# Kernel tuning notes

Hardware: AMD Instinct MI355X
Metric: run time of the kernel (lower is better)

The kernel has to match this reference:

```python
import jax, jax.numpy as jnp
import numpy as np

B, T, ENC_IN, C_OUT = 128, 100, 38, 38
D_MODEL, H, L, D_FF = 512, 8, 3, 512
D_VAE, D_MC, D_C, K = 128, 64, 64, 50
OT_EPS = 0.1

def _ln(x, g, b):
    m = x.mean(-1, keepdims=True)
    v = ((x - m) ** 2).mean(-1, keepdims=True)
    return (x - m) / jnp.sqrt(v + 1e-5) * g + b

def _pos_emb(t, d):
    pos = jnp.arange(t, dtype=jnp.float32)[:, None]
    div = jnp.exp(jnp.arange(0, d, 2, dtype=jnp.float32) * (-np.log(10000.0) / d))
    pe = jnp.zeros((t, d), jnp.float32)
    return pe.at[:, 0::2].set(jnp.sin(pos * div)).at[:, 1::2].set(jnp.cos(pos * div))

def _forward(x, emb_w, Wq, Wk, Wv, Wo, bq, bk, bv, bo, c1w, c1b, c2w, c2b,
             ln1g, ln1b, ln2g, ln2b, lnfg, lnfb, en2de_w, en2de_b,
             eh1w, eh1b, eh2w, eh2b, mamw, mamb, malvw, malvb,
             zmw, zmb, zlvw, zlvb, dzm1w, dzm1b, dzm2w, dzm2b,
             dzl1w, dzl1b, dzl2w, dzl2b, dxm1w, dxm1b, dxm2w, dxm2b,
             otw, otb, theta, projw, projb):
    b, t, _ = x.shape
    # DataEmbedding: circular Conv1d(k=3) token embedding + sinusoidal positions
    xp = jnp.pad(x, ((0, 0), (1, 1), (0, 0)), mode='wrap')
    h = jax.lax.conv_general_dilated(xp, emb_w, (1,), 'VALID',
                                     dimension_numbers=('NWC', 'WIO', 'NWC'))
    h = h + _pos_emb(t, h.shape[-1])[None]
    series_list = []
    scale = 1.0 / jnp.sqrt(jnp.float32(D_MODEL // H))
    for l in range(L):
        q = (h @ Wq[l] + bq[l]).reshape(b, t, H, -1)
        k = (h @ Wk[l] + bk[l]).reshape(b, t, H, -1)
        v = (h @ Wv[l] + bv[l]).reshape(b, t, H, -1)
        # AnomalyAttention series-association: softmax(scale * Q K^T)
        series = jax.nn.softmax(jnp.einsum('bthd,bshd->bhts', q, k) * scale, axis=-1)
        o = jnp.einsum('bhts,bshd->bthd', series, v).reshape(b, t, -1) @ Wo[l] + bo[l]
        h = _ln(h + o, ln1g[l], ln1b[l])
        # conv1d(k=1) FFN == per-token linear; torch weight layout [out, in]
        y = jax.nn.gelu(h @ c1w[l].T + c1b[l], approximate=False) @ c2w[l].T + c2b[l]
        h = _ln(h + y, ln2g[l], ln2b[l])
        series_list.append(series)
    h = _ln(h, lnfg, lnfb)          # encoder final norm
    h = h @ en2de_w + en2de_b       # en2de: [B,T,d_vae]
    # Decoder (eval-mode reparameterization: z = mean)
    h1 = h @ eh1w + eh1b
    h2 = h1 @ eh2w + eh2b
    ma_mean = h2 @ mamw + mamb
    ma_logvar = h2 @ malvw + malvb
    ma = ma_mean
    hb = jnp.concatenate([h1, ma], axis=-1)
    z_mean = hb @ zmw + zmb
    z_logvar = hb @ zlvw + zlvb
    z = z_mean
    # OT concept head: entropic assignment of tokens to concept codebook theta
    pm = ma @ otw + otb             # [B,T,d_c]
    cost = (jnp.sum(pm ** 2, -1, keepdims=True) - 2.0 * (pm @ theta.T)
            + jnp.sum(theta ** 2, -1))   # [B,T,K] squared distances
    p_xj = jax.nn.softmax(-cost / OT_EPS, axis=-1)
    emb = p_xj @ theta              # 'embadding' [B,T,d_c]
    otloss = jnp.mean(jnp.sum(p_xj * cost, -1))
    loss_mse = jnp.mean((emb - pm) ** 2)
    dzm = jax.nn.relu(emb @ dzm1w + dzm1b) @ dzm2w + dzm2b
    dzlv = jax.nn.relu(emb @ dzl1w + dzl1b) @ dzl2w + dzl2b
    dxm = jax.nn.relu(z @ dxm1w + dxm1b) @ dxm2w + dxm2b
    KL_c = jnp.mean(-0.5 * (1.0 - ma_mean ** 2 + ma_logvar - jnp.exp(ma_logvar)))
    qdp = jnp.exp(dzlv - z_logvar)
    KL_z = jnp.mean(0.5 * ((dzm - z_mean) ** 2 / jnp.exp(z_logvar)
                           + qdp - 1.0 - (dzlv - z_logvar)))
    out = (dxm.reshape(b, -1) @ projw + projb).reshape(b, t, -1)
    return out, jnp.stack(series_list), otloss, loss_mse, KL_c, KL_z

def setup_inputs():
    key = jax.random.key(0)
    it = iter(jax.random.split(key, 60))
    p = lambda *s: jax.random.normal(next(it), s, jnp.float32) * 0.02
    return {
        'x': jax.random.normal(next(it), (B, T, ENC_IN), jnp.float32),
        'emb_w': p(3, ENC_IN, D_MODEL),
        'Wq': p(L, D_MODEL, D_MODEL), 'Wk': p(L, D_MODEL, D_MODEL),
        'Wv': p(L, D_MODEL, D_MODEL), 'Wo': p(L, D_MODEL, D_MODEL),
        'bq': p(L, D_MODEL), 'bk': p(L, D_MODEL), 'bv': p(L, D_MODEL), 'bo': p(L, D_MODEL),
        'c1w': p(L, D_FF, D_MODEL), 'c1b': p(L, D_FF),
        'c2w': p(L, D_MODEL, D_FF), 'c2b': p(L, D_MODEL),
        'ln1g': jnp.ones((L, D_MODEL)), 'ln1b': jnp.zeros((L, D_MODEL)),
        'ln2g': jnp.ones((L, D_MODEL)), 'ln2b': jnp.zeros((L, D_MODEL)),
        'lnfg': jnp.ones((D_MODEL,)), 'lnfb': jnp.zeros((D_MODEL,)),
        'en2de_w': p(D_MODEL, D_VAE), 'en2de_b': p(D_VAE),
        'eh1w': p(D_VAE, D_VAE), 'eh1b': p(D_VAE),
        'eh2w': p(D_VAE, D_VAE), 'eh2b': p(D_VAE),
        'mamw': p(D_VAE, D_MC), 'mamb': p(D_MC),
        'malvw': p(D_VAE, D_MC), 'malvb': p(D_MC),
        'zmw': p(D_VAE + D_MC, D_VAE), 'zmb': p(D_VAE),
        'zlvw': p(D_VAE + D_MC, D_VAE), 'zlvb': p(D_VAE),
        'dzm1w': p(D_C, D_VAE), 'dzm1b': p(D_VAE),
        'dzm2w': p(D_VAE, D_VAE), 'dzm2b': p(D_VAE),
        'dzl1w': p(D_C, D_VAE), 'dzl1b': p(D_VAE),
        'dzl2w': p(D_VAE, D_VAE), 'dzl2b': p(D_VAE),
        'dxm1w': p(D_VAE, D_VAE), 'dxm1b': p(D_VAE),
        'dxm2w': p(D_VAE, D_VAE), 'dxm2b': p(D_VAE),
        'otw': p(D_MC, D_C), 'otb': p(D_C),
        'theta': p(K, D_C),
        'projw': p(D_VAE * T, C_OUT * T), 'projb': p(C_OUT * T),
    }

def reference(x, emb_w, Wq, Wk, Wv, Wo, bq, bk, bv, bo, c1w, c1b, c2w, c2b,
              ln1g, ln1b, ln2g, ln2b, lnfg, lnfb, en2de_w, en2de_b,
              eh1w, eh1b, eh2w, eh2b, mamw, mamb, malvw, malvb,
              zmw, zmb, zlvw, zlvb, dzm1w, dzm1b, dzm2w, dzm2b,
              dzl1w, dzl1b, dzl2w, dzl2b, dxm1w, dxm1b, dxm2w, dxm2b,
              otw, otb, theta, projw, projb):
    return _forward(x, emb_w, Wq, Wk, Wv, Wo, bq, bk, bv, bo, c1w, c1b, c2w, c2b,
                    ln1g, ln1b, ln2g, ln2b, lnfg, lnfb, en2de_w, en2de_b,
                    eh1w, eh1b, eh2w, eh2b, mamw, mamb, malvw, malvb,
                    zmw, zmb, zlvw, zlvb, dzm1w, dzm1b, dzm2w, dzm2b,
                    dzl1w, dzl1b, dzl2w, dzl2b, dxm1w, dxm1b, dxm2w, dxm2b,
                    otw, otb, theta, projw, projb)
```

## Files before the change

kernel.cpp:

```cpp
#include <hip/hip_runtime.h>
#include <hip/hip_bf16.h>
#include <math.h>

typedef __hip_bfloat16 bf16;
typedef unsigned int u32;

#define B_      128
#define T_      100
#define ENC_IN_ 38
#define DM_     512
#define H_      8
#define HD_     64
#define L_      3
#define NTOK    (B_*T_)
#define K_CB    50

#define OUT_N     486400
#define SER_N     30720000
#define SER_PER_L 10240000
#define SCALAR_BASE (OUT_N + SER_N)

#define PROJ_KS 16
#define WSEG    786432

__device__ __forceinline__ float ldin(const void* p, size_t i, int f32) {
    if (f32) return ((const float*)p)[i];
    return __bfloat162float(((const bf16*)p)[i]);
}
__device__ __forceinline__ void stout(void* p, size_t i, float v, int f32) {
    if (f32) ((float*)p)[i] = v;
    else     ((bf16*)p)[i] = __float2bfloat16(v);
}

__device__ __forceinline__ ushort bf_hi(float x) {
    union { float f; u32 u; } c; c.f = x;
    return (ushort)((c.u + 0x7FFFu + ((c.u >> 16) & 1u)) >> 16);
}
__device__ __forceinline__ float bf_f(ushort h) {
    union { float f; u32 u; } c; c.u = (u32)h << 16; return c.f;
}

typedef __attribute__((ext_vector_type(8))) short short8v;
typedef __attribute__((ext_vector_type(4))) float f32x4;

__global__ void init_kernel(const void* ln1g, float* acc) {
    if (threadIdx.x < 7) acc[threadIdx.x] = 0.f;
    if (threadIdx.x == 7) {
        u32 w0 = *(const u32*)ln1g;
        ((int*)acc)[7] = (w0 == 0x3F800000u) ? 1 : 0;
    }
}

__launch_bounds__(256)
__global__ void prep_t_kernel(const void* __restrict__ W, const int* __restrict__ flg,
                              ushort* __restrict__ hi, ushort* __restrict__ lo) {
    __shared__ float t[32][33];
    const int k0 = blockIdx.x*32, n0 = blockIdx.y*32, l = blockIdx.z;
    const int c = threadIdx.x & 31, r = threadIdx.x >> 5;
    const int f32 = flg[0];
    const size_t base = (size_t)l*512*512;
#pragma unroll
    for (int i = 0; i < 4; ++i)
        t[r + i*8][c] = ldin(W, base + (size_t)(k0 + r + i*8)*512 + n0 + c, f32);
    __syncthreads();
#pragma unroll
    for (int i = 0; i < 4; ++i) {
        int a = r + i*8;
        float v = t[c][a];
        ushort h = bf_hi(v);
        size_t o = base + (size_t)(n0 + a)*512 + k0 + c;
        hi[o] = h;
        lo[o] = bf_hi(v - bf_f(h));
    }
}

__global__ void prep_s_kernel(const void* __restrict__ W, const int* __restrict__ flg,
                              ushort* __restrict__ hi, ushort* __restrict__ lo, int n) {
    int i = blockIdx.x*256 + threadIdx.x;
    if (i >= n) return;
    float v = ldin(W, i, flg[0]);
    ushort h = bf_hi(v);
    hi[i] = h;
    lo[i] = bf_hi(v - bf_f(h));
}

__launch_bounds__(512)
__global__ void embed_kernel(const void* __restrict__ x, const void* __restrict__ w,
                             const int* __restrict__ flg, float* __restrict__ h) {
    __shared__ float xs[3*ENC_IN_];
    const int f32 = flg[0];
    const int blk = blockIdx.x;
    const int b = blk / T_, t = blk - b*T_;
    const int tid = threadIdx.x;
    if (tid < 3*ENC_IN_) {
        int wv = tid / ENC_IN_, c = tid - wv*ENC_IN_;
        int rr = t - 1 + wv; rr = (rr + T_) % T_;
        xs[tid] = ldin(x, ((size_t)b*T_ + rr)*ENC_IN_ + c, f32);
    }
    __syncthreads();
    int i2 = tid & ~1;
    float freq = expf(-(float)i2 * (9.210340371976184f / 512.f));
    float ang = (float)t * freq;
    float s = (tid & 1) ? cosf(ang) : sinf(ang);
    for (int j = 0; j < 3*ENC_IN_; ++j)
        s = fmaf(xs[j], ldin(w, (size_t)j*DM_ + tid, f32), s);
    h[(size_t)blk*DM_ + tid] = s;
}

#define PK 40
template<int ACT>
__launch_bounds__(256, 1)
__global__ void gemm_mfma_kernel(const float* __restrict__ A,
                                 const ushort* __restrict__ Bh,
                                 const ushort* __restrict__ Bl,
                                 const void* __restrict__ bias, size_t biasoff,
                                 const int* __restrict__ flg,
                                 float* __restrict__ C, int M, int N, int K) {
    __shared__ ushort sAh[128*PK];
    __shared__ ushort sAl[128*PK];
    __shared__ ushort sBh[128*PK];
    __shared__ ushort sBl[128*PK];
    const int tid = threadIdx.x;
    const int lane = tid & 63, wid = tid >> 6;
    const int wr = wid >> 1, wc = wid & 1;
    const int m0 = blockIdx.y * 128, n0 = blockIdx.x * 128;
    const int useBl = flg[0];
    const int r  = tid >> 1;
    const int ks = (tid & 1) * 16;
    const float*  Ap  = A  + (size_t)(m0 + r)*K + ks;
    const ushort* Bhp = Bh + (size_t)(n0 + r)*K + ks;
    const ushort* Blp = Bl + (size_t)(n0 + r)*K + ks;
    const int frow = lane & 15, fk = (lane >> 4) * 8;
    const f32x4 zero = {0.f, 0.f, 0.f, 0.f};
    f32x4 acc[4][4];
#pragma unroll
    for (int m = 0; m < 4; ++m)
#pragma unroll
        for (int n = 0; n < 4; ++n) acc[m][n] = zero;

    for (int k0 = 0; k0 < K; k0 += 32) {
#pragma unroll
        for (int j = 0; j < 4; ++j) {
            float4 v = *(const float4*)(Ap + k0 + j*4);
            ushort4 hi, lo;
            hi.x = bf_hi(v.x); lo.x = bf_hi(v.x - bf_f(hi.x));
            hi.y = bf_hi(v.y); lo.y = bf_hi(v.y - bf_f(hi.y));
            hi.z = bf_hi(v.z); lo.z = bf_hi(v.z - bf_f(hi.z));
            hi.w = bf_hi(v.w); lo.w = bf_hi(v.w - bf_f(hi.w));
            *(ushort4*)&sAh[r*PK + ks + j*4] = hi;
            *(ushort4*)&sAl[r*PK + ks + j*4] = lo;
        }
        *(uint4*)&sBh[r*PK + ks]     = *(const uint4*)(Bhp + k0);
        *(uint4*)&sBh[r*PK + ks + 8] = *(const uint4*)(Bhp + k0 + 8);
        if (useBl) {
            *(uint4*)&sBl[r*PK + ks]     = *(const uint4*)(Blp + k0);
            *(uint4*)&sBl[r*PK + ks + 8] = *(const uint4*)(Blp + k0 + 8);
        }
        __syncthreads();
        short8v ah[4], al[4], bh[4];
#pragma unroll
        for (int m = 0; m < 4; ++m) {
            int row = wr*64 + m*16 + frow;
            ah[m] = *(const short8v*)&sAh[row*PK + fk];
            al[m] = *(const short8v*)&sAl[row*PK + fk];
        }
#pragma unroll
        for (int n = 0; n < 4; ++n) {
            int col = wc*64 + n*16 + frow;
            bh[n] = *(const short8v*)&sBh[col*PK + fk];
        }
#pragma unroll
        for (int m = 0; m < 4; ++m)
#pragma unroll
            for (int n = 0; n < 4; ++n) {
                acc[m][n] = __builtin_amdgcn_mfma_f32_16x16x32_bf16(ah[m], bh[n], acc[m][n], 0, 0, 0);
                acc[m][n] = __builtin_amdgcn_mfma_f32_16x16x32_bf16(al[m], bh[n], acc[m][n], 0, 0, 0);
            }
        if (useBl) {
            short8v bl[4];
#pragma unroll
            for (int n = 0; n < 4; ++n) {
                int col = wc*64 + n*16 + frow;
                bl[n] = *(const short8v*)&sBl[col*PK + fk];
            }
#pragma unroll
            for (int m = 0; m < 4; ++m)
#pragma unroll
                for (int n = 0; n < 4; ++n)
                    acc[m][n] = __builtin_amdgcn_mfma_f32_16x16x32_bf16(ah[m], bl[n], acc[m][n], 0, 0, 0);
        }
        __syncthreads();
    }
    const int f32b = flg[0];
#pragma unroll
    for (int m = 0; m < 4; ++m) {
        int row0 = m0 + wr*64 + m*16 + (lane >> 4)*4;
#pragma unroll
        for (int n = 0; n < 4; ++n) {
            int col = n0 + wc*64 + n*16 + (lane & 15);
            float bv = bias ? ldin(bias, biasoff + col, f32b) : 0.f;
#pragma unroll
            for (int i = 0; i < 4; ++i) {
                float vv = acc[m][n][i] + bv;
                if (ACT == 1) vv = 0.5f*vv*(1.f + erff(vv*0.7071067811865475f));
                C[(size_t)(row0 + i)*N + col] = vv;
            }
        }
    }
}

template<int ACT, int TRANSB>
__launch_bounds__(256)
__global__ void gemm_kernel(const float* __restrict__ A, const void* __restrict__ Bw,
                            size_t bwoff, const void* __restrict__ bias, size_t biasoff,
                            const int* __restrict__ flg,
                            float* __restrict__ C, int M, int N, int K) {
    __shared__ float As[16][68];
    __shared__ float Bs[16][68];
    const int f32 = flg[0];
    const int tid = threadIdx.x;
    const int tx = tid & 15, ty = tid >> 4;
    const int m0 = blockIdx.y * 64, n0 = blockIdx.x * 64;
    float acc[4][4] = {};
    for (int k0 = 0; k0 < K; k0 += 16) {
        for (int i = tid; i < 1024; i += 256) {
            int r = i >> 4, kk = i & 15;
            int gm = m0 + r, gk = k0 + kk;
            As[kk][r] = (gm < M && gk < K) ? A[(size_t)gm*K + gk] : 0.f;
        }
        for (int i = tid; i < 1024; i += 256) {
            int kk, c;
            if (TRANSB) { c = i >> 4; kk = i & 15; }
            else        { kk = i >> 6; c = i & 63; }
            int gk = k0 + kk, gn = n0 + c;
            float vv = 0.f;
            if (gk < K && gn < N)
                vv = TRANSB ? ldin(Bw, bwoff + (size_t)gn*K + gk, f32)
                            : ldin(Bw, bwoff + (size_t)gk*N + gn, f32);
            Bs[kk][c] = vv;
        }
        __syncthreads();
#pragma unroll
        for (int kk = 0; kk < 16; ++kk) {
            float4 av = *(const float4*)&As[kk][ty*4];
            float4 bv = *(const float4*)&Bs[kk][tx*4];
            float a[4] = {av.x, av.y, av.z, av.w};
            float b[4] = {bv.x, bv.y, bv.z, bv.w};
#pragma unroll
            for (int ii = 0; ii < 4; ++ii)
#pragma unroll
                for (int jj = 0; jj < 4; ++jj)
                    acc[ii][jj] = fmaf(a[ii], b[jj], acc[ii][jj]);
        }
        __syncthreads();
    }
#pragma unroll
    for (int ii = 0; ii < 4; ++ii) {
        int gm = m0 + ty*4 + ii;
        if (gm >= M) continue;
#pragma unroll
        for (int jj = 0; jj < 4; ++jj) {
            int gn = n0 + tx*4 + jj;
            if (gn >= N) continue;
            float vv = acc[ii][jj] + (bias ? ldin(bias, biasoff + gn, f32) : 0.f);
            if (ACT == 1) vv = 0.5f * vv * (1.f + erff(vv * 0.7071067811865475f));
            if (ACT == 2) vv = fmaxf(vv, 0.f);
            C[(size_t)gm*N + gn] = vv;
        }
    }
}

__launch_bounds__(256)
__global__ void proj_init_kernel(const void* __restrict__ bias,
                                 const int* __restrict__ flg,
                                 float* __restrict__ C) {
    int i = blockIdx.x*256 + threadIdx.x;
    if (i < OUT_N) C[i] = ldin(bias, (size_t)(i % 3800), flg[0]);
}

__launch_bounds__(256)
__global__ void proj_gemm_kernel(const float* __restrict__ A, const void* __restrict__ Bw,
                                 const int* __restrict__ flg, float* __restrict__ C,
                                 int M, int N, int K, int kchunk) {
    __shared__ float As[16][68];
    __shared__ float Bs[16][68];
    const int f32 = flg[0];
    const int tid = threadIdx.x;
    const int tx = tid & 15, ty = tid >> 4;
    const int m0 = blockIdx.y * 64, n0 = blockIdx.x * 64;
    const int kbeg = blockIdx.z * kchunk;
    const int kend = kbeg + kchunk;
    float acc[4][4] = {};
    for (int k0 = kbeg; k0 < kend; k0 += 16) {
        for (int i = tid; i < 1024; i += 256) {
            int r = i >> 4, kk = i & 15;
            int gm = m0 + r;
            As[kk][r] = (gm < M) ? A[(size_t)gm*K + (k0 + kk)] : 0.f;
        }
        for (int i = tid; i < 1024; i += 256) {
            int kk = i >> 6, c = i & 63;
            int gn = n0 + c;
            Bs[kk][c] = (gn < N) ? ldin(Bw, (size_t)(k0 + kk)*N + gn, f32) : 0.f;
        }
        __syncthreads();
#pragma unroll
        for (int kk = 0; kk < 16; ++kk) {
            float4 av = *(const float4*)&As[kk][ty*4];
            float4 bv = *(const float4*)&Bs[kk][tx*4];
            float a[4] = {av.x, av.y, av.z, av.w};
            float b[4] = {bv.x, bv.y, bv.z, bv.w};
#pragma unroll
            for (int ii = 0; ii < 4; ++ii)
#pragma unroll
                for (int jj = 0; jj < 4; ++jj)
                    acc[ii][jj] = fmaf(a[ii], b[jj], acc[ii][jj]);
        }
        __syncthreads();
    }
#pragma unroll
    for (int ii = 0; ii < 4; ++ii) {
        int gm = m0 + ty*4 + ii;
        if (gm >= M) continue;
#pragma unroll
        for (int jj = 0; jj < 4; ++jj) {
            int gn = n0 + tx*4 + jj;
            if (gn >= N) continue;
            atomicAdd(&C[(size_t)gm*N + gn], acc[ii][jj]);
        }
    }
}

__launch_bounds__(128)
__global__ void series_kernel(const float* __restrict__ Q, const float* __restrict__ Kg,
                              void* __restrict__ outb, size_t soff,
                              const int* __restrict__ flg) {
    __shared__ float qs[64];
    __shared__ float red[128];
    const int t = blockIdx.x, hh = blockIdx.y, b = blockIdx.z;
    const int tid = threadIdx.x;
    const size_t base = (size_t)b*T_*DM_ + (size_t)hh*HD_;
    if (tid < 64) qs[tid] = Q[base + (size_t)t*DM_ + tid];
    __syncthreads();
    float lg = -1e30f;
    if (tid < T_) {
        const float* kr = Kg + base + (size_t)tid*DM_;
        float dot = 0.f;
#pragma unroll 8
        for (int d = 0; d < 64; ++d) dot = fmaf(qs[d], kr[d], dot);
        lg = dot * 0.125f;
    }
    red[tid] = lg;
    __syncthreads();
    for (int st = 64; st > 0; st >>= 1) { if (tid < st) red[tid] = fmaxf(red[tid], red[tid+st]); __syncthreads(); }
    const float mx = red[0];
    __syncthreads();
    float e = (tid < T_) ? expf(lg - mx) : 0.f;
    red[tid] = e;
    __syncthreads();
    for (int st = 64; st > 0; st >>= 1) { if (tid < st) red[tid] += red[tid+st]; __syncthreads(); }
    const float inv = 1.f / red[0];
    if (tid < T_)
        stout(outb, soff + ((size_t)(b*H_ + hh)*T_ + t)*T_ + tid, e * inv, flg[0]);
}

__launch_bounds__(256)
__global__ void attn_kernel(const float* Q, const float* __restrict__ Kg,
                            const float* __restrict__ Vg, float* Cg) {
    __shared__ float Ks[T_*65];
    __shared__ float Vs[T_*65];
    __shared__ float Qrow[4][64];
    __shared__ float Prow[4][104];
    const int tid = threadIdx.x;
    const int lane = tid & 63, w = tid >> 6;
    const int hh = blockIdx.x, b = blockIdx.y;
    const size_t base = (size_t)b*T_*DM_ + (size_t)hh*HD_;
    for (int i = tid; i < T_*HD_; i += 256) {
        int r = i >> 6, d = i & 63;
        size_t g = base + (size_t)r*DM_ + d;
        Ks[r*65+d] = Kg[g];
        Vs[r*65+d] = Vg[g];
    }
    __syncthreads();
    for (int i = 0; i < 25; ++i) {
        const int t = i*4 + w;
        Qrow[w][lane] = Q[base + (size_t)t*DM_ + lane];
        __syncthreads();
        const int s2 = 64 + lane;
        float acc1 = 0.f, acc2 = 0.f;
#pragma unroll 16
        for (int d = 0; d < 64; ++d) {
            float qd = Qrow[w][d];
            acc1 = fmaf(qd, Ks[lane*65 + d], acc1);
            if (s2 < T_) acc2 = fmaf(qd, Ks[s2*65 + d], acc2);
        }
        acc1 *= 0.125f; acc2 *= 0.125f;
        float mx = (s2 < T_) ? fmaxf(acc1, acc2) : acc1;
        for (int off = 32; off > 0; off >>= 1) mx = fmaxf(mx, __shfl_xor(mx, off));
        float e1 = expf(acc1 - mx);
        float e2 = (s2 < T_) ? expf(acc2 - mx) : 0.f;
        float sum = e1 + e2;
        for (int off = 32; off > 0; off >>= 1) sum += __shfl_xor(sum, off);
        float inv = 1.f / sum;
        Prow[w][lane] = e1 * inv;
        if (s2 < T_) Prow[w][s2] = e2 * inv;
        __syncthreads();
        float o = 0.f;
#pragma unroll 10
        for (int s = 0; s < T_; ++s)
            o = fmaf(Prow[w][s], Vs[s*65 + lane], o);
        Cg[base + (size_t)t*DM_ + lane] = o;
    }
}

__launch_bounds__(256)
__global__ void ln_kernel(float* __restrict__ h, const float* __restrict__ res,
                          const void* __restrict__ g, const void* __restrict__ bta,
                          size_t goff, const int* __restrict__ flg) {
    __shared__ float red[256];
    const int f32 = flg[0];
    const int row = blockIdx.x, tid = threadIdx.x;
    float* hp = h + (size_t)row*DM_;
    float x0 = hp[tid], x1 = hp[tid+256];
    if (res) {
        x0 += res[(size_t)row*DM_ + tid];
        x1 += res[(size_t)row*DM_ + tid + 256];
    }
    red[tid] = x0 + x1;
    __syncthreads();
    for (int s = 128; s > 0; s >>= 1) { if (tid < s) red[tid] += red[tid+s]; __syncthreads(); }
    float mean = red[0] * (1.f/512.f);
    __syncthreads();
    float d0 = x0 - mean, d1 = x1 - mean;
    red[tid] = d0*d0 + d1*d1;
    __syncthreads();
    for (int s = 128; s > 0; s >>= 1) { if (tid < s) red[tid] += red[tid+s]; __syncthreads(); }
    float rs = 1.f / sqrtf(red[0]*(1.f/512.f) + 1e-5f);
    hp[tid]     = d0*rs*ldin(g, goff+tid, f32)     + ldin(bta, goff+tid, f32);
    hp[tid+256] = d1*rs*ldin(g, goff+tid+256, f32) + ldin(bta, goff+tid+256, f32);
}

__global__ void concat_kernel(const float* __restrict__ h1, const float* __restrict__ ma,
                              float* __restrict__ hb, int n) {
    int i = blockIdx.x*blockDim.x + threadIdx.x;
    if (i >= n) return;
    int row = i / 192, j = i - row*192;
    hb[i] = (j < 128) ? h1[(size_t)row*128 + j] : ma[(size_t)row*64 + (j-128)];
}

__launch_bounds__(64)
__global__ void ot_kernel(const float* __restrict__ pm, const void* __restrict__ theta,
                          const int* __restrict__ flg,
                          float* __restrict__ embv, float* __restrict__ acc) {
    __shared__ float th[K_CB*64];
    __shared__ float pmv[64];
    __shared__ float red[64];
    __shared__ float pvec[64];
    const int f32 = flg[0];
    const int tid = threadIdx.x;
    const int tok = blockIdx.x;
    for (int i = tid; i < K_CB*64; i += 64) th[i] = ldin(theta, i, f32);
    pmv[tid] = pm[(size_t)tok*64 + tid];
    __syncthreads();
    red[tid] = pmv[tid]*pmv[tid];
    __syncthreads();
    for (int s = 32; s > 0; s >>= 1) { if (tid < s) red[tid] += red[tid+s]; __syncthreads(); }
    float pm2 = red[0];
    __syncthreads();
    float cost = 0.f;
    if (tid < K_CB) {
        const float* tr = th + tid*64;
        float dot = 0.f, t2 = 0.f;
        for (int d = 0; d < 64; ++d) { float tv = tr[d]; dot = fmaf(pmv[d], tv, dot); t2 = fmaf(tv, tv, t2); }
        cost = pm2 - 2.f*dot + t2;
    }
    float logit = (tid < K_CB) ? (-cost / 0.1f) : -1e30f;
    red[tid] = logit;
    __syncthreads();
    for (int s = 32; s > 0; s >>= 1) { if (tid < s) red[tid] = fmaxf(red[tid], red[tid+s]); __syncthreads(); }
    float mx = red[0];
    __syncthreads();
    float e = (tid < K_CB) ? expf(logit - mx) : 0.f;
    red[tid] = e;
    __syncthreads();
    for (int s = 32; s > 0; s >>= 1) { if (tid < s) red[tid] += red[tid+s]; __syncthreads(); }
    float p = e / red[0];
    __syncthreads();
    pvec[tid] = p;
    red[tid] = p * cost;
    __syncthreads();
    for (int s = 32; s > 0; s >>= 1) { if (tid < s) red[tid] += red[tid+s]; __syncthreads(); }
    if (tid == 0) atomicAdd(acc + 0, red[0]);
    __syncthreads();
    float eb = 0.f;
    for (int kk = 0; kk < K_CB; ++kk) eb = fmaf(pvec[kk], th[kk*64 + tid], eb);
    embv[(size_t)tok*64 + tid] = eb;
    float dd = eb - pmv[tid];
    red[tid] = dd*dd;
    __syncthreads();
    for (int s = 32; s > 0; s >>= 1) { if (tid < s) red[tid] += red[tid+s]; __syncthreads(); }
    if (tid == 0) atomicAdd(acc + 1, red[0]);
}

__global__ void klc_kernel(const float* __restrict__ m, const float* __restrict__ lv,
                           float* __restrict__ acc) {
    __shared__ float red[256];
    const int tid = threadIdx.x;
    float s = 0.f;
    for (int i = blockIdx.x*256 + tid; i < NTOK*64; i += gridDim.x*256) {
        float mm = m[i], l = lv[i];
        s += -0.5f * (1.f - mm*mm + l - expf(l));
    }
    red[tid] = s; __syncthreads();
    for (int st = 128; st > 0; st >>= 1) { if (tid < st) red[tid] += red[tid+st]; __syncthreads(); }
    if (tid == 0) atomicAdd(acc + 2, red[0]);
}

__global__ void klz_kernel(const float* __restrict__ dzm, const float* __restrict__ zm,
                           const float* __restrict__ zlv, const float* __restrict__ dzl,
                           float* __restrict__ acc) {
    __shared__ float red[256];
    const int tid = threadIdx.x;
    float s = 0.f;
    for (int i = blockIdx.x*256 + tid; i < NTOK*128; i += gridDim.x*256) {
        float d = dzm[i] - zm[i];
        float zl = zlv[i], dl = dzl[i];
        s += 0.5f * (d*d / expf(zl) + expf(dl - zl) - 1.f - (dl - zl));
    }
    red[tid] = s; __syncthreads();
    for (int st = 128; st > 0; st >>= 1) { if (tid < st) red[tid] += red[tid+st]; __syncthreads(); }
    if (tid == 0) atomicAdd(acc + 3, red[0]);
}

__global__ void finalize_kernel(const float* __restrict__ outf, const float* __restrict__ acc,
                                void* __restrict__ outb) {
    const int f32 = ((const int*)acc)[7];
    int i = blockIdx.x*blockDim.x + threadIdx.x;
    if (i < OUT_N) stout(outb, i, outf[i], f32);
    if (i == 0) {
        stout(outb, SCALAR_BASE + 0, acc[0] * (1.f/12800.f),   f32);
        stout(outb, SCALAR_BASE + 1, acc[1] * (1.f/819200.f),  f32);
        stout(outb, SCALAR_BASE + 2, acc[2] * (1.f/819200.f),  f32);
        stout(outb, SCALAR_BASE + 3, acc[3] * (1.f/1638400.f), f32);
    }
}

static inline void launch_gemm(hipStream_t st, int act, int transb,
                               const float* A, const void* Bw, size_t bwoff,
                               const void* bias, size_t biasoff,
                               const int* flg, float* C, int M, int N, int K) {
    dim3 g((N + 63)/64, (M + 63)/64);
    if      (act == 0 && !transb) gemm_kernel<0,0><<<g,256,0,st>>>(A,Bw,bwoff,bias,biasoff,flg,C,M,N,K);
    else if (act == 0 &&  transb) gemm_kernel<0,1><<<g,256,0,st>>>(A,Bw,bwoff,bias,biasoff,flg,C,M,N,K);
    else if (act == 1)            gemm_kernel<1,1><<<g,256,0,st>>>(A,Bw,bwoff,bias,biasoff,flg,C,M,N,K);
    else                          gemm_kernel<2,0><<<g,256,0,st>>>(A,Bw,bwoff,bias,biasoff,flg,C,M,N,K);
}

extern "C" void kernel_launch(void* const* d_in, const int* in_sizes, int n_in,
                              void* d_out, int out_size, void* d_ws, size_t ws_size,
                              hipStream_t stream) {
    const void* x      = d_in[0];
    const void* emb_w  = d_in[1];
    const void* Wq     = d_in[2];
    const void* Wk     = d_in[3];
    const void* Wv     = d_in[4];
    const void* Wo     = d_in[5];
    const void* bq     = d_in[6];
    const void* bk     = d_in[7];
    const void* bv     = d_in[8];
    const void* bo     = d_in[9];
    const void* c1w    = d_in[10];
    const void* c1b    = d_in[11];
    const void* c2w    = d_in[12];
    const void* c2b    = d_in[13];
    const void* ln1g   = d_in[14];
    const void* ln1b   = d_in[15];
    const void* ln2g   = d_in[16];
    const void* ln2b   = d_in[17];
    const void* lnfg   = d_in[18];
    const void* lnfb   = d_in[19];
    const void* en2de_w= d_in[20];
    const void* en2de_b= d_in[21];
    const void* eh1w   = d_in[22];
    const void* eh1b   = d_in[23];
    const void* eh2w   = d_in[24];
    const void* eh2b   = d_in[25];
    const void* mamw   = d_in[26];
    const void* mamb   = d_in[27];
    const void* malvw  = d_in[28];
    const void* malvb  = d_in[29];
    const void* zmw    = d_in[30];
    const void* zmb    = d_in[31];
    const void* zlvw   = d_in[32];
    const void* zlvb   = d_in[33];
    const void* dzm1w  = d_in[34];
    const void* dzm1b  = d_in[35];
    const void* dzm2w  = d_in[36];
    const void* dzm2b  = d_in[37];
    const void* dzl1w  = d_in[38];
    const void* dzl1b  = d_in[39];
    const void* dzl2w  = d_in[40];
    const void* dzl2b  = d_in[41];
    const void* dxm1w  = d_in[42];
    const void* dxm1b  = d_in[43];
    const void* dxm2w  = d_in[44];
    const void* dxm2b  = d_in[45];
    const void* otw    = d_in[46];
    const void* otb    = d_in[47];
    const void* theta  = d_in[48];
    const void* projw  = d_in[49];
    const void* projb  = d_in[50];

    float* ws = (float*)d_ws;
    const size_t NBUF = (size_t)NTOK * DM_;
    float* acc = ws;
    const int* flg = (const int*)ws + 7;
    float* h  = ws + 16;
    float* q  = h + NBUF;
    float* kb = h + 2*NBUF;
    float* vb = h + 3*NBUF;
    float* hv    = q;
    float* h1    = q  + 1638400;
    float* h2    = q  + 3276800;
    float* ma    = q  + 4915200;
    float* malv  = q  + 5734400;
    float* hb    = kb;
    float* zmean = kb + 2457600;
    float* zlvB  = kb + 4096000;
    float* pmb   = kb + 5734400;
    float* embv  = vb;
    float* t1    = vb + 819200;
    float* dzmB  = vb + 2457600;
    float* dzlB  = vb + 4096000;
    float* dxmB  = h;
    float* outf  = h + 1638400;
    ushort* wp  = (ushort*)(vb + NBUF);
    ushort* wqh = wp;            ushort* wql = wp + 1*(size_t)WSEG;
    ushort* wkh = wp + 2*(size_t)WSEG;   ushort* wkl = wp + 3*(size_t)WSEG;
    ushort* wvh = wp + 4*(size_t)WSEG;   ushort* wvl = wp + 5*(size_t)WSEG;
    ushort* woh = wp + 6*(size_t)WSEG;   ushort* wol = wp + 7*(size_t)WSEG;
    ushort* c1h = wp + 8*(size_t)WSEG;   ushort* c1l = wp + 9*(size_t)WSEG;
    ushort* c2h = wp + 10*(size_t)WSEG;  ushort* c2l = wp + 11*(size_t)WSEG;

    init_kernel<<<1, 64, 0, stream>>>(ln1g, acc);
    {
        dim3 tg(16, 16, 3);
        prep_t_kernel<<<tg, 256, 0, stream>>>(Wq, flg, wqh, wql);
        prep_t_kernel<<<tg, 256, 0, stream>>>(Wk, flg, wkh, wkl);
        prep_t_kernel<<<tg, 256, 0, stream>>>(Wv, flg, wvh, wvl);
        prep_t_kernel<<<tg, 256, 0, stream>>>(Wo, flg, woh, wol);
        prep_s_kernel<<<(WSEG + 255)/256, 256, 0, stream>>>(c1w, flg, c1h, c1l, WSEG);
        prep_s_kernel<<<(WSEG + 255)/256, 256, 0, stream>>>(c2w, flg, c2h, c2l, WSEG);
    }
    embed_kernel<<<NTOK, 512, 0, stream>>>(x, emb_w, flg, h);

    const dim3 mg(4, 100);
    for (int l = 0; l < L_; ++l) {
        const size_t PW = (size_t)l * DM_ * DM_;
        const size_t BOFF = (size_t)l * DM_;
        gemm_mfma_kernel<0><<<mg, 256, 0, stream>>>(h, wqh+PW, wql+PW, bq, BOFF, flg, q,  NTOK, DM_, DM_);
        gemm_mfma_kernel<0><<<mg, 256, 0, stream>>>(h, wkh+PW, wkl+PW, bk, BOFF, flg, kb, NTOK, DM_, DM_);
        gemm_mfma_kernel<0><<<mg, 256, 0, stream>>>(h, wvh+PW, wvl+PW, bv, BOFF, flg, vb, NTOK, DM_, DM_);
        dim3 sg(T_, H_, B_);
        series_kernel<<<sg, 128, 0, stream>>>(q, kb, d_out,
            (size_t)OUT_N + (size_t)l * SER_PER_L, flg);
        dim3 ag(H_, B_);
        attn_kernel<<<ag, 256, 0, stream>>>(q, kb, vb, q);
        gemm_mfma_kernel<0><<<mg, 256, 0, stream>>>(q, woh+PW, wol+PW, bo, BOFF, flg, kb, NTOK, DM_, DM_);
        ln_kernel<<<NTOK, 256, 0, stream>>>(h, kb, ln1g, ln1b, BOFF, flg);
        gemm_mfma_kernel<1><<<mg, 256, 0, stream>>>(h, c1h+PW, c1l+PW, c1b, BOFF, flg, q,  NTOK, DM_, DM_);
        gemm_mfma_kernel<0><<<mg, 256, 0, stream>>>(q, c2h+PW, c2l+PW, c2b, BOFF, flg, kb, NTOK, DM_, DM_);
        ln_kernel<<<NTOK, 256, 0, stream>>>(h, kb, ln2g, ln2b, BOFF, flg);
    }
    ln_kernel<<<NTOK, 256, 0, stream>>>(h, nullptr, lnfg, lnfb, 0, flg);

    launch_gemm(stream, 0, 0, h,  en2de_w, 0, en2de_b, 0, flg, hv, NTOK, 128, 512);
    launch_gemm(stream, 0, 0, hv, eh1w, 0, eh1b, 0, flg, h1, NTOK, 128, 128);
    launch_gemm(stream, 0, 0, h1, eh2w, 0, eh2b, 0, flg, h2, NTOK, 128, 128);
    launch_gemm(stream, 0, 0, h2, mamw, 0, mamb, 0, flg, ma,   NTOK, 64, 128);
    launch_gemm(stream, 0, 0, h2, malvw, 0, malvb, 0, flg, malv, NTOK, 64, 128);
    concat_kernel<<<(NTOK*192 + 255)/256, 256, 0, stream>>>(h1, ma, hb, NTOK*192);
    launch_gemm(stream, 0, 0, hb, zmw, 0, zmb, 0, flg, zmean, NTOK, 128, 192);
    launch_gemm(stream, 0, 0, hb, zlvw, 0, zlvb, 0, flg, zlvB,  NTOK, 128, 192);
    launch_gemm(stream, 0, 0, ma, otw, 0, otb, 0, flg, pmb, NTOK, 64, 64);
    ot_kernel<<<NTOK, 64, 0, stream>>>(pmb, theta, flg, embv, acc);
    launch_gemm(stream, 2, 0, embv, dzm1w, 0, dzm1b, 0, flg, t1, NTOK, 128, 64);
    launch_gemm(stream, 0, 0, t1, dzm2w, 0, dzm2b, 0, flg, dzmB, NTOK, 128, 128);
    launch_gemm(stream, 2, 0, embv, dzl1w, 0, dzl1b, 0, flg, t1, NTOK, 128, 64);
    launch_gemm(stream, 0, 0, t1, dzl2w, 0, dzl2b, 0, flg, dzlB, NTOK, 128, 128);
    launch_gemm(stream, 2, 0, zmean, dxm1w, 0, dxm1b, 0, flg, t1, NTOK, 128, 128);
    launch_gemm(stream, 0, 0, t1, dxm2w, 0, dxm2b, 0, flg, dxmB, NTOK, 128, 128);
    klc_kernel<<<256, 256, 0, stream>>>(ma, malv, acc);
    klz_kernel<<<256, 256, 0, stream>>>(dzmB, zmean, zlvB, dzlB, acc);
    proj_init_kernel<<<(OUT_N + 255)/256, 256, 0, stream>>>(projb, flg, outf);
    {
        dim3 pg((3800 + 63)/64, (B_ + 63)/64, PROJ_KS);
        proj_gemm_kernel<<<pg, 256, 0, stream>>>(dxmB, projw, flg, outf,
                                                 B_, 3800, 12800, 12800/PROJ_KS);
    }
    finalize_kernel<<<(OUT_N + 255)/256, 256, 0, stream>>>(outf, acc, d_out);
}
```

Baseline: 4.412 ms.

## Fuse series softmax output into attention kernel and widen projection GEMM tiles

The separate series_kernel, which recomputed QK^T and softmax per query row, is removed. attn_kernel now writes the normalized attention probabilities straight to the series output, so each layer skips one launch and a second pass over Q and K. The projection GEMM now computes a 64x128 tile per block with 8 columns per thread, and the split-K factor doubles to keep enough blocks. Risks are more register pressure in the projection kernel and more atomic contention from the doubled split-K.

```diff
diff --git a/kernel.cpp b/kernel.cpp
--- a/kernel.cpp
+++ b/kernel.cpp
@@ -20,7 +20,7 @@
 #define SER_PER_L 10240000
 #define SCALAR_BASE (OUT_N + SER_N)
 
-#define PROJ_KS 16
+#define PROJ_KS 32
 #define WSEG    786432
 
 __device__ __forceinline__ float ldin(const void* p, size_t i, int f32) {
@@ -283,22 +283,22 @@
                                  const int* __restrict__ flg, float* __restrict__ C,
                                  int M, int N, int K, int kchunk) {
     __shared__ float As[16][68];
-    __shared__ float Bs[16][68];
+    __shared__ float Bs[16][132];
     const int f32 = flg[0];
     const int tid = threadIdx.x;
     const int tx = tid & 15, ty = tid >> 4;
-    const int m0 = blockIdx.y * 64, n0 = blockIdx.x * 64;
+    const int m0 = blockIdx.y * 64, n0 = blockIdx.x * 128;
     const int kbeg = blockIdx.z * kchunk;
     const int kend = kbeg + kchunk;
-    float acc[4][4] = {};
+    float acc[4][8] = {};
     for (int k0 = kbeg; k0 < kend; k0 += 16) {
         for (int i = tid; i < 1024; i += 256) {
             int r = i >> 4, kk = i & 15;
             int gm = m0 + r;
             As[kk][r] = (gm < M) ? A[(size_t)gm*K + (k0 + kk)] : 0.f;
         }
-        for (int i = tid; i < 1024; i += 256) {
-            int kk = i >> 6, c = i & 63;
+        for (int i = tid; i < 2048; i += 256) {
+            int kk = i >> 7, c = i & 127;
             int gn = n0 + c;
             Bs[kk][c] = (gn < N) ? ldin(Bw, (size_t)(k0 + kk)*N + gn, f32) : 0.f;
         }
@@ -306,13 +306,14 @@
 #pragma unroll
         for (int kk = 0; kk < 16; ++kk) {
             float4 av = *(const float4*)&As[kk][ty*4];
-            float4 bv = *(const float4*)&Bs[kk][tx*4];
+            float4 b0 = *(const float4*)&Bs[kk][tx*8];
+            float4 b1 = *(const float4*)&Bs[kk][tx*8 + 4];
             float a[4] = {av.x, av.y, av.z, av.w};
-            float b[4] = {bv.x, bv.y, bv.z, bv.w};
+            float b[8] = {b0.x,b0.y,b0.z,b0.w,b1.x,b1.y,b1.z,b1.w};
 #pragma unroll
             for (int ii = 0; ii < 4; ++ii)
 #pragma unroll
-                for (int jj = 0; jj < 4; ++jj)
+                for (int jj = 0; jj < 8; ++jj)
                     acc[ii][jj] = fmaf(a[ii], b[jj], acc[ii][jj]);
         }
         __syncthreads();
@@ -322,50 +323,19 @@
         int gm = m0 + ty*4 + ii;
         if (gm >= M) continue;
 #pragma unroll
-        for (int jj = 0; jj < 4; ++jj) {
-            int gn = n0 + tx*4 + jj;
+        for (int jj = 0; jj < 8; ++jj) {
+            int gn = n0 + tx*8 + jj;
             if (gn >= N) continue;
             atomicAdd(&C[(size_t)gm*N + gn], acc[ii][jj]);
         }
     }
 }
 
-__launch_bounds__(128)
-__global__ void series_kernel(const float* __restrict__ Q, const float* __restrict__ Kg,
-                              void* __restrict__ outb, size_t soff,
-                              const int* __restrict__ flg) {
-    __shared__ float qs[64];
-    __shared__ float red[128];
-    const int t = blockIdx.x, hh = blockIdx.y, b = blockIdx.z;
-    const int tid = threadIdx.x;
-    const size_t base = (size_t)b*T_*DM_ + (size_t)hh*HD_;
-    if (tid < 64) qs[tid] = Q[base + (size_t)t*DM_ + tid];
-    __syncthreads();
-    float lg = -1e30f;
-    if (tid < T_) {
-        const float* kr = Kg + base + (size_t)tid*DM_;
-        float dot = 0.f;
-#pragma unroll 8
-        for (int d = 0; d < 64; ++d) dot = fmaf(qs[d], kr[d], dot);
-        lg = dot * 0.125f;
-    }
-    red[tid] = lg;
-    __syncthreads();
-    for (int st = 64; st > 0; st >>= 1) { if (tid < st) red[tid] = fmaxf(red[tid], red[tid+st]); __syncthreads(); }
-    const float mx = red[0];
-    __syncthreads();
-    float e = (tid < T_) ? expf(lg - mx) : 0.f;
-    red[tid] = e;
-    __syncthreads();
-    for (int st = 64; st > 0; st >>= 1) { if (tid < st) red[tid] += red[tid+st]; __syncthreads(); }
-    const float inv = 1.f / red[0];
-    if (tid < T_)
-        stout(outb, soff + ((size_t)(b*H_ + hh)*T_ + t)*T_ + tid, e * inv, flg[0]);
-}
-
 __launch_bounds__(256)
 __global__ void attn_kernel(const float* Q, const float* __restrict__ Kg,
-                            const float* __restrict__ Vg, float* Cg) {
+                            const float* __restrict__ Vg, float* Cg,
+                            void* __restrict__ outb, size_t soff,
+                            const int* __restrict__ flg) {
     __shared__ float Ks[T_*65];
     __shared__ float Vs[T_*65];
     __shared__ float Qrow[4][64];
@@ -373,6 +343,7 @@
     const int tid = threadIdx.x;
     const int lane = tid & 63, w = tid >> 6;
     const int hh = blockIdx.x, b = blockIdx.y;
+    const int f32o = flg[0];
     const size_t base = (size_t)b*T_*DM_ + (size_t)hh*HD_;
     for (int i = tid; i < T_*HD_; i += 256) {
         int r = i >> 6, d = i & 63;
@@ -401,8 +372,12 @@
         float sum = e1 + e2;
         for (int off = 32; off > 0; off >>= 1) sum += __shfl_xor(sum, off);
         float inv = 1.f / sum;
-        Prow[w][lane] = e1 * inv;
-        if (s2 < T_) Prow[w][s2] = e2 * inv;
+        float p1 = e1 * inv, p2 = e2 * inv;
+        size_t sb = soff + ((size_t)(b*H_ + hh)*T_ + t)*T_;
+        stout(outb, sb + lane, p1, f32o);
+        if (s2 < T_) stout(outb, sb + s2, p2, f32o);
+        Prow[w][lane] = p1;
+        if (s2 < T_) Prow[w][s2] = p2;
         __syncthreads();
         float o = 0.f;
 #pragma unroll 10
@@ -660,11 +635,9 @@
         gemm_mfma_kernel<0><<<mg, 256, 0, stream>>>(h, wqh+PW, wql+PW, bq, BOFF, flg, q,  NTOK, DM_, DM_);
         gemm_mfma_kernel<0><<<mg, 256, 0, stream>>>(h, wkh+PW, wkl+PW, bk, BOFF, flg, kb, NTOK, DM_, DM_);
         gemm_mfma_kernel<0><<<mg, 256, 0, stream>>>(h, wvh+PW, wvl+PW, bv, BOFF, flg, vb, NTOK, DM_, DM_);
-        dim3 sg(T_, H_, B_);
-        series_kernel<<<sg, 128, 0, stream>>>(q, kb, d_out,
+        dim3 ag(H_, B_);
+        attn_kernel<<<ag, 256, 0, stream>>>(q, kb, vb, q, d_out,
             (size_t)OUT_N + (size_t)l * SER_PER_L, flg);
-        dim3 ag(H_, B_);
-        attn_kernel<<<ag, 256, 0, stream>>>(q, kb, vb, q);
         gemm_mfma_kernel<0><<<mg, 256, 0, stream>>>(q, woh+PW, wol+PW, bo, BOFF, flg, kb, NTOK, DM_, DM_);
         ln_kernel<<<NTOK, 256, 0, stream>>>(h, kb, ln1g, ln1b, BOFF, flg);
         gemm_mfma_kernel<1><<<mg, 256, 0, stream>>>(h, c1h+PW, c1l+PW, c1b, BOFF, flg, q,  NTOK, DM_, DM_);
@@ -693,7 +666,7 @@
     klz_kernel<<<256, 256, 0, stream>>>(dzmB, zmean, zlvB, dzlB, acc);
     proj_init_kernel<<<(OUT_N + 255)/256, 256, 0, stream>>>(projb, flg, outf);
     {
-        dim3 pg((3800 + 63)/64, (B_ + 63)/64, PROJ_KS);
+        dim3 pg((3800 + 127)/128, (B_ + 63)/64, PROJ_KS);
         proj_gemm_kernel<<<pg, 256, 0, stream>>>(dxmB, projw, flg, outf,
                                                  B_, 3800, 12800, 12800/PROJ_KS);
     }
```

Measured after the change: 3.679 ms. -16.6%, faster.
